# Kernel tuning notes

Measured on AMD Instinct MI355X. Metric: run time of the kernel, lower is better.

The kernel has to match this reference:

```python
import jax, jax.numpy as jnp
import numpy as np

M = 65536  # total flattened feature length (sum of ragged segment lengths n_k)
K = 4096   # number of segments (sub-networks)
B = 256    # batch size


def setup_inputs() -> dict:
    key = jax.random.key(0)
    k1, k2, k3 = jax.random.split(key, 3)
    x = jax.random.normal(k1, (B, 1, M), dtype=jnp.float32)
    w = jax.random.normal(k2, (M,), dtype=jnp.float32)
    # contiguous ragged segments: sorted segment ids in [0, K)
    seg_ids = jnp.sort(jax.random.randint(k3, (M,), 0, K, dtype=jnp.int32))
    return {"x": x, "w": w, "seg_ids": seg_ids, "num_segments": K}


def reference(x, w, seg_ids, num_segments):
    # GINN input layer: for each batch row, slice the flat input into K ragged
    # contiguous segments, dot each segment with the matching slice of the flat
    # weight vector, concatenate the K scalars, apply tanh.
    # Equivalent fused form: u2[b,k] = sum_{i in seg k} w[i]*x[b,0,i]; out = tanh(u2)
    xs = x[:, 0, :]                      # [B, M]
    prod = xs * w                        # [B, M] elementwise
    seg_sum = jax.vmap(
        lambda p: jax.ops.segment_sum(p, seg_ids, num_segments=num_segments)
    )(prod)                              # [B, K]
    return jnp.tanh(seg_sum)
```

## Files before the change

### kernel.cpp

```cpp
#include <hip/hip_runtime.h>


#define TPB   256
#define WIN   1024
#define EPL   16
#define ROWS  8
#define RPW   2
#define SLOTS 192

__global__ __launch_bounds__(TPB) void zero_out_k(float* __restrict__ out, int n4) {
    int i = blockIdx.x * blockDim.x + threadIdx.x;
    if (i < n4) reinterpret_cast<float4*>(out)[i] = make_float4(0.f, 0.f, 0.f, 0.f);
}

__global__ __launch_bounds__(TPB) void seg_window_acc(
        const float* __restrict__ x,
        const float* __restrict__ w,
        const int*   __restrict__ ids,
        float* __restrict__ out,
        float* __restrict__ carry,
        int M, int K, int NW) {
    __shared__ float slab[ROWS][SLOTS];

    const int t   = threadIdx.x;
    const int ln  = t & 63;
    const int wv  = t >> 6;
    const int win = blockIdx.x;
    const int r0  = blockIdx.y * ROWS;
    const size_t mbase = (size_t)win * WIN + (size_t)ln * EPL;

    const int4*   id4 = reinterpret_cast<const int4*>(ids + mbase);
    const float4* w4  = reinterpret_cast<const float4*>(w + mbase);
    int4   i0 = id4[0], i1 = id4[1], i2 = id4[2], i3 = id4[3];
    float4 q0 = w4[0],  q1 = w4[1],  q2 = w4[2],  q3 = w4[3];

    const int rowA = r0 + wv * RPW;
    const int rowB = rowA + 1;
    const float4* xa4 = reinterpret_cast<const float4*>(x + (size_t)rowA * M + mbase);
    const float4* xb4 = reinterpret_cast<const float4*>(x + (size_t)rowB * M + mbase);
    float4 a0 = xa4[0], a1 = xa4[1], a2 = xa4[2], a3 = xa4[3];
    float4 c0 = xb4[0], c1 = xb4[1], c2 = xb4[2], c3 = xb4[3];

    #pragma unroll
    for (int i = t; i < ROWS * SLOTS; i += TPB) (&slab[0][0])[i] = 0.f;
    __syncthreads();

    const int firstId = __shfl(i0.x, 0);
    const int lastId  = __shfl(i3.w, 63);

    float* __restrict__ rsA = slab[wv * RPW + 0];
    float* __restrict__ rsB = slab[wv * RPW + 1];

    float accA = 0.f, accB = 0.f;
    int prev = i0.x;

    #define STEP(idv, xav, xbv, wvv)                                   \
        if ((idv) != prev) {                                           \
            int s = min(prev - firstId, SLOTS - 1);                    \
            atomicAdd(&rsA[s], accA);                                  \
            atomicAdd(&rsB[s], accB);                                  \
            accA = 0.f; accB = 0.f; prev = (idv);                      \
        }                                                              \
        accA = fmaf((xav), (wvv), accA);                               \
        accB = fmaf((xbv), (wvv), accB);

    STEP(i0.x, a0.x, c0.x, q0.x)  STEP(i0.y, a0.y, c0.y, q0.y)
    STEP(i0.z, a0.z, c0.z, q0.z)  STEP(i0.w, a0.w, c0.w, q0.w)
    STEP(i1.x, a1.x, c1.x, q1.x)  STEP(i1.y, a1.y, c1.y, q1.y)
    STEP(i1.z, a1.z, c1.z, q1.z)  STEP(i1.w, a1.w, c1.w, q1.w)
    STEP(i2.x, a2.x, c2.x, q2.x)  STEP(i2.y, a2.y, c2.y, q2.y)
    STEP(i2.z, a2.z, c2.z, q2.z)  STEP(i2.w, a2.w, c2.w, q2.w)
    STEP(i3.x, a3.x, c3.x, q3.x)  STEP(i3.y, a3.y, c3.y, q3.y)
    STEP(i3.z, a3.z, c3.z, q3.z)  STEP(i3.w, a3.w, c3.w, q3.w)
    #undef STEP
    {
        int s = min(prev - firstId, SLOTS - 1);
        atomicAdd(&rsA[s], accA);
        atomicAdd(&rsB[s], accB);
    }
    __syncthreads();

    const int span = min(lastId - firstId + 1, SLOTS);
    for (int i = t; i < ROWS * span; i += TPB) {
        int rr = i / span;
        int s  = i - rr * span;
        int id = firstId + s;
        int row = r0 + rr;
        float v = slab[rr][s];
        if (s == 0)
            carry[((size_t)row * NW + win) * 2 + 0] = v;
        else if (id == lastId)
            carry[((size_t)row * NW + win) * 2 + 1] = v;
        else
            out[(size_t)row * K + id] = tanhf(v);
    }
}

__global__ __launch_bounds__(TPB) void seg_fixup(
        const int*   __restrict__ ids,
        const float* __restrict__ carry,
        float* __restrict__ out,
        int K, int NW, int B) {
    int t = blockIdx.x * blockDim.x + threadIdx.x;
    if (t >= B * NW) return;
    int row = t / NW;
    int win = t - row * NW;

    int firstId = ids[win * WIN];
    int lastId  = ids[win * WIN + WIN - 1];
    float cF = carry[((size_t)row * NW + win) * 2 + 0];
    float cL = carry[((size_t)row * NW + win) * 2 + 1];

    int prevLast = (win > 0) ? ids[win * WIN - 1] : -1;
    if (prevLast != firstId)
        out[(size_t)row * K + firstId] = tanhf(cF);

    float tot = cL;
    if (win + 1 < NW) {
        int nextFirst = ids[(win + 1) * WIN];
        if (nextFirst == lastId)
            tot += carry[((size_t)row * NW + win + 1) * 2 + 0];
    }
    out[(size_t)row * K + lastId] = tanhf(tot);
}

extern "C" void kernel_launch(void* const* d_in, const int* in_sizes, int n_in,
                              void* d_out, int out_size, void* d_ws, size_t ws_size,
                              hipStream_t stream) {
    const float* x       = (const float*)d_in[0];
    const float* w       = (const float*)d_in[1];
    const int*   seg_ids = (const int*)d_in[2];
    float* out = (float*)d_out;

    const int M = in_sizes[1];
    const int B = in_sizes[0] / M;
    const int K = out_size / B;
    const int NW = M / WIN;

    float* carry = (float*)d_ws;

    const int n4 = out_size / 4;
    zero_out_k<<<(n4 + TPB - 1) / TPB, TPB, 0, stream>>>(out, n4);

    dim3 grid(NW, B / ROWS);
    seg_window_acc<<<grid, TPB, 0, stream>>>(x, w, seg_ids, out, carry, M, K, NW);

    const int nfix = B * NW;
    seg_fixup<<<(nfix + TPB - 1) / TPB, TPB, 0, stream>>>(seg_ids, carry, out, K, NW, B);
}
```

Before: 29.52 us.

## Make windows wave-independent and loop over row pairs with prefetch of next rows

```diff
diff --git a/kernel.cpp b/kernel.cpp
--- a/kernel.cpp
+++ b/kernel.cpp
@@ -4,95 +4,114 @@
 #define TPB   256
 #define WIN   1024
 #define EPL   16
-#define ROWS  8
-#define RPW   2
 #define SLOTS 192
+#define ITERS 4
 
 __global__ __launch_bounds__(TPB) void zero_out_k(float* __restrict__ out, int n4) {
     int i = blockIdx.x * blockDim.x + threadIdx.x;
     if (i < n4) reinterpret_cast<float4*>(out)[i] = make_float4(0.f, 0.f, 0.f, 0.f);
 }
 
-__global__ __launch_bounds__(TPB) void seg_window_acc(
+__global__ __launch_bounds__(TPB) void seg_persist(
         const float* __restrict__ x,
         const float* __restrict__ w,
         const int*   __restrict__ ids,
         float* __restrict__ out,
         float* __restrict__ carry,
-        int M, int K, int NW) {
-    __shared__ float slab[ROWS][SLOTS];
+        int M, int K, int NW, int B) {
+    __shared__ float slab[TPB / 64][2][SLOTS];
 
-    const int t   = threadIdx.x;
-    const int ln  = t & 63;
-    const int wv  = t >> 6;
-    const int win = blockIdx.x;
-    const int r0  = blockIdx.y * ROWS;
+    const int ln  = threadIdx.x & 63;
+    const int wv  = threadIdx.x >> 6;
+    const int wid = blockIdx.x * (TPB / 64) + wv;
+    const int win = wid % NW;
+    const int grp = wid / NW;
+    const int bp0 = grp * ITERS;
     const size_t mbase = (size_t)win * WIN + (size_t)ln * EPL;
+    const int halfB = B / 2;
 
     const int4*   id4 = reinterpret_cast<const int4*>(ids + mbase);
     const float4* w4  = reinterpret_cast<const float4*>(w + mbase);
     int4   i0 = id4[0], i1 = id4[1], i2 = id4[2], i3 = id4[3];
     float4 q0 = w4[0],  q1 = w4[1],  q2 = w4[2],  q3 = w4[3];
 
-    const int rowA = r0 + wv * RPW;
-    const int rowB = rowA + 1;
-    const float4* xa4 = reinterpret_cast<const float4*>(x + (size_t)rowA * M + mbase);
-    const float4* xb4 = reinterpret_cast<const float4*>(x + (size_t)rowB * M + mbase);
-    float4 a0 = xa4[0], a1 = xa4[1], a2 = xa4[2], a3 = xa4[3];
-    float4 c0 = xb4[0], c1 = xb4[1], c2 = xb4[2], c3 = xb4[3];
+    const int firstId = __shfl(i0.x, 0);
+    const int lastId  = __shfl(i3.w, 63);
+    const int span    = min(lastId - firstId + 1, SLOTS);
+
+    float* __restrict__ sA = slab[wv][0];
+    float* __restrict__ sB = slab[wv][1];
+
+    float4 aC[4], cC[4], aN[4], cN[4];
+    {
+        const float4* xa4 = reinterpret_cast<const float4*>(x + (size_t)bp0 * M + mbase);
+        const float4* xb4 = reinterpret_cast<const float4*>(x + (size_t)(bp0 + halfB) * M + mbase);
+        aC[0] = xa4[0]; aC[1] = xa4[1]; aC[2] = xa4[2]; aC[3] = xa4[3];
+        cC[0] = xb4[0]; cC[1] = xb4[1]; cC[2] = xb4[2]; cC[3] = xb4[3];
+    }
 
     #pragma unroll
-    for (int i = t; i < ROWS * SLOTS; i += TPB) (&slab[0][0])[i] = 0.f;
-    __syncthreads();
+    for (int it = 0; it < ITERS; ++it) {
+        const int bp  = bp0 + it;
+        const int bpn = bp0 + ((it + 1 < ITERS) ? (it + 1) : it);
+        {
+            const float4* xa4 = reinterpret_cast<const float4*>(x + (size_t)bpn * M + mbase);
+            const float4* xb4 = reinterpret_cast<const float4*>(x + (size_t)(bpn + halfB) * M + mbase);
+            aN[0] = xa4[0]; aN[1] = xa4[1]; aN[2] = xa4[2]; aN[3] = xa4[3];
+            cN[0] = xb4[0]; cN[1] = xb4[1]; cN[2] = xb4[2]; cN[3] = xb4[3];
+        }
+        #pragma unroll
+        for (int i = ln; i < 2 * SLOTS; i += 64) (&sA[0])[i] = 0.f;
+        asm volatile("s_waitcnt lgkmcnt(0)" ::: "memory");
+        __builtin_amdgcn_sched_barrier(0);
 
-    const int firstId = __shfl(i0.x, 0);
-    const int lastId  = __shfl(i3.w, 63);
+        float accA = 0.f, accB = 0.f;
+        int prev = i0.x;
+        #define STEP(idv, xav, xbv, wvv)                               \
+            if ((idv) != prev) {                                       \
+                int s = min(prev - firstId, SLOTS - 1);                \
+                atomicAdd(&sA[s], accA);                               \
+                atomicAdd(&sB[s], accB);                               \
+                accA = 0.f; accB = 0.f; prev = (idv);                  \
+            }                                                          \
+            accA = fmaf((xav), (wvv), accA);                           \
+            accB = fmaf((xbv), (wvv), accB);
 
-    float* __restrict__ rsA = slab[wv * RPW + 0];
-    float* __restrict__ rsB = slab[wv * RPW + 1];
+        STEP(i0.x, aC[0].x, cC[0].x, q0.x)  STEP(i0.y, aC[0].y, cC[0].y, q0.y)
+        STEP(i0.z, aC[0].z, cC[0].z, q0.z)  STEP(i0.w, aC[0].w, cC[0].w, q0.w)
+        STEP(i1.x, aC[1].x, cC[1].x, q1.x)  STEP(i1.y, aC[1].y, cC[1].y, q1.y)
+        STEP(i1.z, aC[1].z, cC[1].z, q1.z)  STEP(i1.w, aC[1].w, cC[1].w, q1.w)
+        STEP(i2.x, aC[2].x, cC[2].x, q2.x)  STEP(i2.y, aC[2].y, cC[2].y, q2.y)
+        STEP(i2.z, aC[2].z, cC[2].z, q2.z)  STEP(i2.w, aC[2].w, cC[2].w, q2.w)
+        STEP(i3.x, aC[3].x, cC[3].x, q3.x)  STEP(i3.y, aC[3].y, cC[3].y, q3.y)
+        STEP(i3.z, aC[3].z, cC[3].z, q3.z)  STEP(i3.w, aC[3].w, cC[3].w, q3.w)
+        #undef STEP
+        {
+            int s = min(prev - firstId, SLOTS - 1);
+            atomicAdd(&sA[s], accA);
+            atomicAdd(&sB[s], accB);
+        }
+        asm volatile("s_waitcnt lgkmcnt(0)" ::: "memory");
+        __builtin_amdgcn_sched_barrier(0);
 
-    float accA = 0.f, accB = 0.f;
-    int prev = i0.x;
+        for (int i = ln; i < 2 * span; i += 64) {
+            int rr  = (i >= span) ? 1 : 0;
+            int s   = i - rr * span;
+            int id  = firstId + s;
+            int row = rr ? (bp + halfB) : bp;
+            float v = slab[wv][rr][s];
+            if (s == 0)
+                carry[((size_t)row * NW + win) * 2 + 0] = v;
+            else if (id == lastId)
+                carry[((size_t)row * NW + win) * 2 + 1] = v;
+            else
+                out[(size_t)row * K + id] = tanhf(v);
+        }
+        asm volatile("s_waitcnt lgkmcnt(0)" ::: "memory");
+        __builtin_amdgcn_sched_barrier(0);
 
-    #define STEP(idv, xav, xbv, wvv)                                   \
-        if ((idv) != prev) {                                           \
-            int s = min(prev - firstId, SLOTS - 1);                    \
-            atomicAdd(&rsA[s], accA);                                  \
-            atomicAdd(&rsB[s], accB);                                  \
-            accA = 0.f; accB = 0.f; prev = (idv);                      \
-        }                                                              \
-        accA = fmaf((xav), (wvv), accA);                               \
-        accB = fmaf((xbv), (wvv), accB);
-
-    STEP(i0.x, a0.x, c0.x, q0.x)  STEP(i0.y, a0.y, c0.y, q0.y)
-    STEP(i0.z, a0.z, c0.z, q0.z)  STEP(i0.w, a0.w, c0.w, q0.w)
-    STEP(i1.x, a1.x, c1.x, q1.x)  STEP(i1.y, a1.y, c1.y, q1.y)
-    STEP(i1.z, a1.z, c1.z, q1.z)  STEP(i1.w, a1.w, c1.w, q1.w)
-    STEP(i2.x, a2.x, c2.x, q2.x)  STEP(i2.y, a2.y, c2.y, q2.y)
-    STEP(i2.z, a2.z, c2.z, q2.z)  STEP(i2.w, a2.w, c2.w, q2.w)
-    STEP(i3.x, a3.x, c3.x, q3.x)  STEP(i3.y, a3.y, c3.y, q3.y)
-    STEP(i3.z, a3.z, c3.z, q3.z)  STEP(i3.w, a3.w, c3.w, q3.w)
-    #undef STEP
-    {
-        int s = min(prev - firstId, SLOTS - 1);
-        atomicAdd(&rsA[s], accA);
-        atomicAdd(&rsB[s], accB);
-    }
-    __syncthreads();
-
-    const int span = min(lastId - firstId + 1, SLOTS);
-    for (int i = t; i < ROWS * span; i += TPB) {
-        int rr = i / span;
-        int s  = i - rr * span;
-        int id = firstId + s;
-        int row = r0 + rr;
-        float v = slab[rr][s];
-        if (s == 0)
-            carry[((size_t)row * NW + win) * 2 + 0] = v;
-        else if (id == lastId)
-            carry[((size_t)row * NW + win) * 2 + 1] = v;
-        else
-            out[(size_t)row * K + id] = tanhf(v);
+        #pragma unroll
+        for (int j = 0; j < 4; ++j) { aC[j] = aN[j]; cC[j] = cN[j]; }
     }
 }
 
@@ -142,8 +161,9 @@
     const int n4 = out_size / 4;
     zero_out_k<<<(n4 + TPB - 1) / TPB, TPB, 0, stream>>>(out, n4);
 
-    dim3 grid(NW, B / ROWS);
-    seg_window_acc<<<grid, TPB, 0, stream>>>(x, w, seg_ids, out, carry, M, K, NW);
+    const int nwaves = NW * ((B / 2) / ITERS);
+    const int nblk   = nwaves / (TPB / 64);
+    seg_persist<<<nblk, TPB, 0, stream>>>(x, w, seg_ids, out, carry, M, K, NW, B);
 
     const int nfix = B * NW;
     seg_fixup<<<(nfix + TPB - 1) / TPB, TPB, 0, stream>>>(seg_ids, carry, out, K, NW, B);
```

Result: slower. 31.24 us (+5.8%).
